# Kernel optimization log

Measured on AMD Instinct MI355X. Metric: run time of the kernel, lower is better.

The kernel has to match this reference:

```python
import jax, jax.numpy as jnp
import numpy as np

KH = KW = 3
K = KH * KW
STRIDE = 1
PAD = 1
DIL = 1
DG = 1  # deformable groups


def conv2d(x, w, b):
    out = jax.lax.conv_general_dilated(
        x, w, window_strides=(STRIDE, STRIDE),
        padding=[(PAD, PAD), (PAD, PAD)], rhs_dilation=(DIL, DIL),
        dimension_numbers=('NCHW', 'OIHW', 'NCHW'))
    return out + b[None, :, None, None]


def deform_conv2d(x, offset, mask, w, b):
    """DCNv2: bilinear sample at predicted offsets, modulate by mask, GEMM with w."""
    B, Cin, H, W = x.shape
    Ho, Wo = offset.shape[2], offset.shape[3]
    cpg = Cin // DG
    # torchvision layout: channel 2*(g*K+k) = dy, 2*(g*K+k)+1 = dx
    off = offset.reshape(B, DG, K, 2, Ho, Wo)
    off_y, off_x = off[:, :, :, 0], off[:, :, :, 1]  # [B,DG,K,Ho,Wo]
    m = mask.reshape(B, DG, K, Ho, Wo)
    ky = jnp.repeat(jnp.arange(KH), KW) * DIL          # [K] kernel row offsets
    kx = jnp.tile(jnp.arange(KW), KH) * DIL            # [K] kernel col offsets
    hh = jnp.arange(Ho) * STRIDE - PAD
    ww = jnp.arange(Wo) * STRIDE - PAD
    py = off_y + ky[None, None, :, None, None] + hh[None, None, None, :, None]
    px = off_x + kx[None, None, :, None, None] + ww[None, None, None, None, :]
    y0 = jnp.floor(py); x0 = jnp.floor(px)
    wy = py - y0; wx = px - x0
    x_g = x.reshape(B, DG, cpg, H * W)

    def gather(yc, xc):  # zero-padded bilinear corner fetch
        valid = ((yc >= 0) & (yc < H) & (xc >= 0) & (xc < W)).astype(x.dtype)
        yi = jnp.clip(yc, 0, H - 1).astype(jnp.int32)
        xi = jnp.clip(xc, 0, W - 1).astype(jnp.int32)
        idx = (yi * W + xi).reshape(B, DG, 1, K * Ho * Wo)
        v = jnp.take_along_axis(x_g, jnp.broadcast_to(idx, (B, DG, cpg, K * Ho * Wo)), axis=3)
        return v.reshape(B, DG, cpg, K, Ho, Wo) * valid[:, :, None]

    v00 = gather(y0, x0)
    v01 = gather(y0, x0 + 1)
    v10 = gather(y0 + 1, x0)
    v11 = gather(y0 + 1, x0 + 1)
    wy_b = wy[:, :, None]; wx_b = wx[:, :, None]  # broadcast over cpg
    sampled = (v00 * (1 - wy_b) * (1 - wx_b) + v01 * (1 - wy_b) * wx_b
               + v10 * wy_b * (1 - wx_b) + v11 * wy_b * wx_b)
    sampled = (sampled * m[:, :, None]).reshape(B, Cin, K, Ho, Wo)
    Cout = w.shape[0]
    out = jnp.einsum('bckhw,ock->bohw', sampled, w.reshape(Cout, Cin, K))
    return out + b[None, :, None, None]


def setup_inputs() -> dict:
    key = jax.random.key(0)
    k1, k2, k3, k4 = jax.random.split(key, 4)
    B, Cin, Cout, H, W = 8, 128, 128, 64, 64
    omc = DG * 3 * K  # 2*K offsets + K mask channels = 27
    x = jax.random.normal(k1, (B, Cin, H, W), dtype=jnp.float32)
    # small offset-conv weights -> modest predicted offsets (mimics near-zero init)
    w_off = jax.random.normal(k2, (omc, Cin, KH, KW), dtype=jnp.float32) * 0.01
    b_off = jnp.zeros((omc,), dtype=jnp.float32)
    w_def = jax.random.normal(k3, (Cout, Cin, KH, KW), dtype=jnp.float32) * (1.0 / np.sqrt(Cin * K))
    b_def = jax.random.normal(k4, (Cout,), dtype=jnp.float32) * 0.01
    return {"x": x, "w_off": w_off, "b_off": b_off, "w_def": w_def, "b_def": b_def}


def reference(x, w_off, b_off, w_def, b_def):
    out = conv2d(x, w_off, b_off)
    oc = DG * 2 * K
    offset = out[:, :oc]
    mask = jax.nn.sigmoid(out[:, oc:])
    return deform_conv2d(x, offset, mask, w_def, b_def)
```

## Files before the change

kernel.cpp:

```cpp
#include <hip/hip_runtime.h>
#include <math.h>

typedef _Float16 f16;
typedef __attribute__((ext_vector_type(2))) _Float16 f16x2;
typedef __attribute__((ext_vector_type(4))) _Float16 f16x4;
typedef __attribute__((ext_vector_type(8))) _Float16 f16x8;
typedef __attribute__((ext_vector_type(4))) float f32x4;

#define NBATCH 8
#define WSA_ELE 36864
#define WSB_ELE 147456
#define PREP_BLOCKS 720
#define OFF_WSB  73728
#define OFF_XT   368640

#define WIN_OFF    0
#define A_OFF      131072
#define SOFF_OFF   147456
#define SMEM_BYTES 161536

__device__ __forceinline__ void gload_lds16(const f16* gsrc, f16* ldst) {
  __builtin_amdgcn_global_load_lds(
      (const __attribute__((address_space(1))) unsigned int*)gsrc,
      (__attribute__((address_space(3))) unsigned int*)ldst, 16, 0, 0);
}

__global__ __launch_bounds__(256) void prep_transpose_kernel(const float* __restrict__ w_off,
                                                             const float* __restrict__ w_def,
                                                             f16* __restrict__ wsA,
                                                             f16* __restrict__ wsB,
                                                             const float* __restrict__ x,
                                                             f16* __restrict__ xt) {
  __shared__ __align__(16) f16 s_t[128 * 68];
  const int t = threadIdx.x;
  if (blockIdx.x < PREP_BLOCKS) {
    int i = blockIdx.x * 256 + t;
    if (i < WSA_ELE) {
      int j = i & 7, lane = (i >> 3) & 63, fm = i >> 9;
      int ch = fm >> 1, mt = fm & 1;
      int row = mt * 16 + (lane & 15);
      int kidx = ch * 32 + (lane >> 4) * 8 + j;
      int k = kidx >> 7, cc = kidx & 127;
      float v = (row < 27) ? w_off[row * 1152 + cc * 9 + k] : 0.0f;
      wsA[i] = (f16)v;
    } else {
      int e = i - WSA_ELE;
      int j = e & 7, lane = (e >> 3) & 63, fm = e >> 9;
      int ch = fm >> 3, mt = fm & 7;
      int row = mt * 16 + (lane & 15);
      int kidx = ch * 32 + (lane >> 4) * 8 + j;
      int k = kidx >> 7, cc = kidx & 127;
      wsB[e] = (f16)w_def[row * 1152 + cc * 9 + k];
    }
    return;
  }
  const int bid = blockIdx.x - PREP_BLOCKS;
  const int b = bid >> 6;
  const int pos0 = (bid & 63) << 6;
  const float* xb = x + ((size_t)b << 19);
  #pragma unroll
  for (int it = 0; it < 8; ++it) {
    int i = it * 256 + t;
    int c = i >> 4, p4 = (i & 15) << 2;
    float4 v = *(const float4*)&xb[c * 4096 + pos0 + p4];
    f16x4 h = {(f16)v.x, (f16)v.y, (f16)v.z, (f16)v.w};
    *(f16x4*)&s_t[c * 68 + p4] = h;
  }
  __syncthreads();
  f16* xtb = xt + ((size_t)b << 19);
  #pragma unroll
  for (int it = 0; it < 8; ++it) {
    int i = it * 256 + t;
    int p = i >> 5, c4 = (i & 31) << 2;
    f16x4 h = {s_t[(c4    ) * 68 + p],
               s_t[(c4 + 1) * 68 + p],
               s_t[(c4 + 2) * 68 + p],
               s_t[(c4 + 3) * 68 + p]};
    *(f16x4*)&xtb[(size_t)(pos0 + p) * 128 + c4] = h;
  }
}

__global__ __launch_bounds__(512, 1) void fused_dcn_kernel(const f16* __restrict__ xt,
                                                           const f16* __restrict__ wsA,
                                                           const f16* __restrict__ wsB,
                                                           const float* __restrict__ b_off,
                                                           const float* __restrict__ b_def,
                                                           float* __restrict__ out) {
  extern __shared__ __align__(16) char smem[];
  char*  win      = smem;
  f16*   s_a      = (f16*)(smem + A_OFF);
  float* s_offall = (float*)(smem + SOFF_OFF);

  const int t = threadIdx.x;
  const int b = blockIdx.x & 7;
  const int hp = blockIdx.x >> 3;
  const int lane = t & 63, wid = t >> 6;
  const int row = wid >> 2;
  const int rowy = hp * 2 + row;
  const int q = lane >> 4, li = lane & 15;
  const int px = ((wid & 3) << 4) + li;
  const char* xtb = (const char*)xt + ((size_t)b << 20);
  const int y_lo = max(hp * 2 - 3, 0);
  const int y_hi = min(hp * 2 + 4, 63);

  {
    const int nunits = (y_hi - y_lo + 1) << 10;
    for (int u = t; u < nunits; u += 512) {
      const int r = u >> 10, rem = u & 1023;
      const int xx = rem >> 4, s = rem & 15;
      const int qq = s & 3, cc4 = s >> 2;
      const uint4 v = *(const uint4*)(xtb + ((((y_lo + r) * 64 + xx) << 8) + (cc4 << 6) + (qq << 4)));
      const int s1 = xx & 3, s2 = (xx >> 2) & 1;
      *(uint4*)(win + (((r * 64 + xx) << 8) + ((qq ^ s1) << 4) + ((cc4 ^ s2) << 6))) = v;
    }
  }
  __syncthreads();

  {
    float* so = s_offall + row * (27 * 65);
    f32x4 acc0 = {0.f, 0.f, 0.f, 0.f}, acc1 = {0.f, 0.f, 0.f, 0.f};
    #pragma unroll
    for (int k = 0; k < 9; ++k) {
      const int ky = k / 3, kx = k - ky * 3;
      const int y = rowy + ky - 1;
      const int xx = px + kx - 1;
      const bool valid = ((unsigned)y < 64u) && ((unsigned)xx < 64u);
      const int yc = min(max(y, y_lo), y_hi);
      const int xc = min(max(xx, 0), 63);
      const int base = (((yc - y_lo) * 64 + xc) << 8) + ((q ^ (xc & 3)) << 4) + ((((xc >> 2) & 1)) << 6);
      #pragma unroll
      for (int c4 = 0; c4 < 4; ++c4) {
        union { uint4 u; f16x8 v; } bu;
        bu.u = *(const uint4*)(win + (base ^ (c4 << 6)));
        if (!valid) { bu.u.x = 0u; bu.u.y = 0u; bu.u.z = 0u; bu.u.w = 0u; }
        const int ch = k * 4 + c4;
        f16x8 a0 = *(const f16x8*)&wsA[(ch * 2    ) * 512 + lane * 8];
        f16x8 a1 = *(const f16x8*)&wsA[(ch * 2 + 1) * 512 + lane * 8];
        acc0 = __builtin_amdgcn_mfma_f32_16x16x32_f16(a0, bu.v, acc0, 0, 0, 0);
        acc1 = __builtin_amdgcn_mfma_f32_16x16x32_f16(a1, bu.v, acc1, 0, 0, 0);
      }
    }
    #pragma unroll
    for (int mt = 0; mt < 2; ++mt) {
      f32x4 a = mt ? acc1 : acc0;
      #pragma unroll
      for (int r = 0; r < 4; ++r) {
        int oc = mt * 16 + q * 4 + r;
        if (oc < 27) {
          float v = a[r] + b_off[oc];
          if (oc >= 18) v = 1.0f / (1.0f + __expf(-v));
          so[oc * 65 + px] = v;
        }
      }
    }
  }
  __syncthreads();

  unsigned posA[9], posB[9];
  f16x4 wts[9];
  {
    const float* so = s_offall + row * (27 * 65);
    #pragma unroll
    for (int k = 0; k < 9; ++k) {
      const int ky = k / 3, kx = k - ky * 3;
      float oy = so[(2 * k    ) * 65 + px];
      float ox = so[(2 * k + 1) * 65 + px];
      float m  = so[(18 + k   ) * 65 + px];
      float py  = oy + (float)(rowy + ky - 1);
      float pxf = ox + (float)(px + kx - 1);
      float y0f = floorf(py), x0f = floorf(pxf);
      float wy = py - y0f, wx = pxf - x0f;
      int y0 = (int)y0f, x0 = (int)x0f;
      bool y0v = (unsigned)y0 < 64u, y1v = (unsigned)(y0 + 1) < 64u;
      bool x0v = (unsigned)x0 < 64u, x1v = (unsigned)(x0 + 1) < 64u;
      int y0a = min(max(y0, y_lo), y_hi), y1a = min(max(y0 + 1, y_lo), y_hi);
      int x0c = min(max(x0, 0), 63),      x1c = min(max(x0 + 1, 0), 63);
      unsigned i00 = (unsigned)((y0a - y_lo) * 64 + x0c);
      unsigned i01 = (unsigned)((y0a - y_lo) * 64 + x1c);
      unsigned i10 = (unsigned)((y1a - y_lo) * 64 + x0c);
      unsigned i11 = (unsigned)((y1a - y_lo) * 64 + x1c);
      posA[k] = i00 | (i01 << 16);
      posB[k] = i10 | (i11 << 16);
      float w0 = (y0v && x0v) ? (1.f - wy) * (1.f - wx) * m : 0.f;
      float w1 = (y0v && x1v) ? (1.f - wy) * wx         * m : 0.f;
      float w2 = (y1v && x0v) ? wy         * (1.f - wx) * m : 0.f;
      float w3 = (y1v && x1v) ? wy         * wx         * m : 0.f;
      f16x4 wp = {(f16)w0, (f16)w1, (f16)w2, (f16)w3};
      wts[k] = wp;
    }
  }

  gload_lds16(wsB + wid * 512 + lane * 8, s_a + wid * 512);
  __syncthreads();

  f32x4 acc[8];
  #pragma unroll
  for (int mt = 0; mt < 8; ++mt) acc[mt] = (f32x4){0.f, 0.f, 0.f, 0.f};

  #pragma unroll
  for (int k = 0; k < 9; ++k) {
    const unsigned wA = posA[k], wB = posB[k];
    const unsigned i00 = wA & 0xFFFFu, i01 = wA >> 16;
    const unsigned i10 = wB & 0xFFFFu, i11 = wB >> 16;
    const int b00 = (int)((i00 << 8) + (((unsigned)q ^ (i00 & 3)) << 4) + (((i00 >> 2) & 1) << 6));
    const int b01 = (int)((i01 << 8) + (((unsigned)q ^ (i01 & 3)) << 4) + (((i01 >> 2) & 1) << 6));
    const int b10 = (int)((i10 << 8) + (((unsigned)q ^ (i10 & 3)) << 4) + (((i10 >> 2) & 1) << 6));
    const int b11 = (int)((i11 << 8) + (((unsigned)q ^ (i11 & 3)) << 4) + (((i11 >> 2) & 1) << 6));
    const f16x4 wv = wts[k];
    const f16x2 wp0 = {wv.x, wv.x}, wp1 = {wv.y, wv.y};
    const f16x2 wp2 = {wv.z, wv.z}, wp3 = {wv.w, wv.w};
    #pragma unroll
    for (int c4 = 0; c4 < 4; ++c4) {
      const int ch = k * 4 + c4;
      if (ch < 35)
        gload_lds16(wsB + (ch + 1) * 4096 + wid * 512 + lane * 8,
                    s_a + ((ch + 1) & 1) * 4096 + wid * 512);
      const int cx = c4 << 6;
      union { uint4 u; f16x2 h[4]; } d0, d1, d2, d3;
      d0.u = *(const uint4*)(win + (b00 ^ cx));
      d1.u = *(const uint4*)(win + (b01 ^ cx));
      d2.u = *(const uint4*)(win + (b10 ^ cx));
      d3.u = *(const uint4*)(win + (b11 ^ cx));
      union { f16x2 h[4]; f16x8 v; } bf;
      #pragma unroll
      for (int i = 0; i < 4; ++i) {
        f16x2 s = d0.h[i] * wp0;
        s = s + d1.h[i] * wp1;
        s = s + d2.h[i] * wp2;
        s = s + d3.h[i] * wp3;
        bf.h[i] = s;
      }
      const f16* ab = s_a + (ch & 1) * 4096;
      #pragma unroll
      for (int mt = 0; mt < 8; ++mt) {
        f16x8 a = *(const f16x8*)&ab[mt * 512 + lane * 8];
        acc[mt] = __builtin_amdgcn_mfma_f32_16x16x32_f16(a, bf.v, acc[mt], 0, 0, 0);
      }
      __syncthreads();
    }
  }

  float* o = out + (size_t)b * 128 * 4096 + rowy * 64 + px;
  #pragma unroll
  for (int mt = 0; mt < 8; ++mt) {
    #pragma unroll
    for (int r = 0; r < 4; ++r) {
      int oc = mt * 16 + q * 4 + r;
      o[oc * 4096] = acc[mt][r] + b_def[oc];
    }
  }
}

extern "C" void kernel_launch(void* const* d_in, const int* in_sizes, int n_in,
                              void* d_out, int out_size, void* d_ws, size_t ws_size,
                              hipStream_t stream) {
  const float* x     = (const float*)d_in[0];
  const float* w_off = (const float*)d_in[1];
  const float* b_off = (const float*)d_in[2];
  const float* w_def = (const float*)d_in[3];
  const float* b_def = (const float*)d_in[4];
  float* out = (float*)d_out;

  f16* wsA = (f16*)d_ws;
  f16* wsB = (f16*)((char*)d_ws + OFF_WSB);
  f16* xt  = (f16*)((char*)d_ws + OFF_XT);

  static int smem_opted = 0;
  if (!smem_opted) {
    hipFuncSetAttribute((const void*)fused_dcn_kernel,
                        hipFuncAttributeMaxDynamicSharedMemorySize, SMEM_BYTES);
    smem_opted = 1;
  }

  prep_transpose_kernel<<<dim3(PREP_BLOCKS + NBATCH * 64), dim3(256), 0, stream>>>(
      w_off, w_def, wsA, wsB, x, xt);
  fused_dcn_kernel<<<dim3(NBATCH * 32), dim3(512), SMEM_BYTES, stream>>>(
      xt, wsA, wsB, b_off, b_def, out);
}
```

Measured before the change: 111.7 us.

## Fuse NCHW-to-NHWC fp16 transpose into main DCN kernel window load

Removes the separate x transpose pass and its global fp16 intermediate. The main kernel now reads fp32 NCHW rows directly, converts them to fp16, and transposes them through an LDS scratch tile into the swizzled window. The scratch region is shared with the offset buffer and the weight staging area to cut LDS use, which needs an extra barrier. The cost is that each block re-reads and re-transposes up to 8 overlapping rows, and each row goes through two barriers serially with little overlap.

```diff
diff --git a/kernel.cpp b/kernel.cpp
--- a/kernel.cpp
+++ b/kernel.cpp
@@ -12,12 +12,10 @@
 #define WSB_ELE 147456
 #define PREP_BLOCKS 720
 #define OFF_WSB  73728
-#define OFF_XT   368640
 
 #define WIN_OFF    0
-#define A_OFF      131072
-#define SOFF_OFF   147456
-#define SMEM_BYTES 161536
+#define SCR_OFF    131072
+#define SMEM_BYTES 148480
 
 __device__ __forceinline__ void gload_lds16(const f16* gsrc, f16* ldst) {
   __builtin_amdgcn_global_load_lds(
@@ -25,71 +23,41 @@
       (__attribute__((address_space(3))) unsigned int*)ldst, 16, 0, 0);
 }
 
-__global__ __launch_bounds__(256) void prep_transpose_kernel(const float* __restrict__ w_off,
-                                                             const float* __restrict__ w_def,
-                                                             f16* __restrict__ wsA,
-                                                             f16* __restrict__ wsB,
-                                                             const float* __restrict__ x,
-                                                             f16* __restrict__ xt) {
-  __shared__ __align__(16) f16 s_t[128 * 68];
-  const int t = threadIdx.x;
-  if (blockIdx.x < PREP_BLOCKS) {
-    int i = blockIdx.x * 256 + t;
-    if (i < WSA_ELE) {
-      int j = i & 7, lane = (i >> 3) & 63, fm = i >> 9;
-      int ch = fm >> 1, mt = fm & 1;
-      int row = mt * 16 + (lane & 15);
-      int kidx = ch * 32 + (lane >> 4) * 8 + j;
-      int k = kidx >> 7, cc = kidx & 127;
-      float v = (row < 27) ? w_off[row * 1152 + cc * 9 + k] : 0.0f;
-      wsA[i] = (f16)v;
-    } else {
-      int e = i - WSA_ELE;
-      int j = e & 7, lane = (e >> 3) & 63, fm = e >> 9;
-      int ch = fm >> 3, mt = fm & 7;
-      int row = mt * 16 + (lane & 15);
-      int kidx = ch * 32 + (lane >> 4) * 8 + j;
-      int k = kidx >> 7, cc = kidx & 127;
-      wsB[e] = (f16)w_def[row * 1152 + cc * 9 + k];
-    }
-    return;
-  }
-  const int bid = blockIdx.x - PREP_BLOCKS;
-  const int b = bid >> 6;
-  const int pos0 = (bid & 63) << 6;
-  const float* xb = x + ((size_t)b << 19);
-  #pragma unroll
-  for (int it = 0; it < 8; ++it) {
-    int i = it * 256 + t;
-    int c = i >> 4, p4 = (i & 15) << 2;
-    float4 v = *(const float4*)&xb[c * 4096 + pos0 + p4];
-    f16x4 h = {(f16)v.x, (f16)v.y, (f16)v.z, (f16)v.w};
-    *(f16x4*)&s_t[c * 68 + p4] = h;
-  }
-  __syncthreads();
-  f16* xtb = xt + ((size_t)b << 19);
-  #pragma unroll
-  for (int it = 0; it < 8; ++it) {
-    int i = it * 256 + t;
-    int p = i >> 5, c4 = (i & 31) << 2;
-    f16x4 h = {s_t[(c4    ) * 68 + p],
-               s_t[(c4 + 1) * 68 + p],
-               s_t[(c4 + 2) * 68 + p],
-               s_t[(c4 + 3) * 68 + p]};
-    *(f16x4*)&xtb[(size_t)(pos0 + p) * 128 + c4] = h;
-  }
-}
-
-__global__ __launch_bounds__(512, 1) void fused_dcn_kernel(const f16* __restrict__ xt,
+__global__ __launch_bounds__(256) void prep_w_kernel(const float* __restrict__ w_off,
+                                                     const float* __restrict__ w_def,
+                                                     f16* __restrict__ wsA,
+                                                     f16* __restrict__ wsB) {
+  int i = blockIdx.x * 256 + threadIdx.x;
+  if (i < WSA_ELE) {
+    int j = i & 7, lane = (i >> 3) & 63, fm = i >> 9;
+    int ch = fm >> 1, mt = fm & 1;
+    int row = mt * 16 + (lane & 15);
+    int kidx = ch * 32 + (lane >> 4) * 8 + j;
+    int k = kidx >> 7, cc = kidx & 127;
+    float v = (row < 27) ? w_off[row * 1152 + cc * 9 + k] : 0.0f;
+    wsA[i] = (f16)v;
+  } else {
+    int e = i - WSA_ELE;
+    int j = e & 7, lane = (e >> 3) & 63, fm = e >> 9;
+    int ch = fm >> 3, mt = fm & 7;
+    int row = mt * 16 + (lane & 15);
+    int kidx = ch * 32 + (lane >> 4) * 8 + j;
+    int k = kidx >> 7, cc = kidx & 127;
+    wsB[e] = (f16)w_def[row * 1152 + cc * 9 + k];
+  }
+}
+
+__global__ __launch_bounds__(512, 1) void fused_dcn_kernel(const float* __restrict__ x,
                                                            const f16* __restrict__ wsA,
                                                            const f16* __restrict__ wsB,
                                                            const float* __restrict__ b_off,
                                                            const float* __restrict__ b_def,
                                                            float* __restrict__ out) {
   extern __shared__ __align__(16) char smem[];
-  char*  win      = smem;
-  f16*   s_a      = (f16*)(smem + A_OFF);
-  float* s_offall = (float*)(smem + SOFF_OFF);
+  char*  win      = smem + WIN_OFF;
+  f16*   tile     = (f16*)(smem + SCR_OFF);
+  float* s_offall = (float*)(smem + SCR_OFF);
+  f16*   s_a      = (f16*)(smem + SCR_OFF);
 
   const int t = threadIdx.x;
   const int b = blockIdx.x & 7;
@@ -99,22 +67,35 @@
   const int rowy = hp * 2 + row;
   const int q = lane >> 4, li = lane & 15;
   const int px = ((wid & 3) << 4) + li;
-  const char* xtb = (const char*)xt + ((size_t)b << 20);
   const int y_lo = max(hp * 2 - 3, 0);
   const int y_hi = min(hp * 2 + 4, 63);
-
-  {
-    const int nunits = (y_hi - y_lo + 1) << 10;
-    for (int u = t; u < nunits; u += 512) {
-      const int r = u >> 10, rem = u & 1023;
-      const int xx = rem >> 4, s = rem & 15;
-      const int qq = s & 3, cc4 = s >> 2;
-      const uint4 v = *(const uint4*)(xtb + ((((y_lo + r) * 64 + xx) << 8) + (cc4 << 6) + (qq << 4)));
-      const int s1 = xx & 3, s2 = (xx >> 2) & 1;
-      *(uint4*)(win + (((r * 64 + xx) << 8) + ((qq ^ s1) << 4) + ((cc4 ^ s2) << 6))) = v;
-    }
-  }
-  __syncthreads();
+  const int nrows = y_hi - y_lo + 1;
+  const float* xb = x + ((size_t)b << 19);
+
+  for (int rr = 0; rr < nrows; ++rr) {
+    const int y = y_lo + rr;
+    #pragma unroll
+    for (int i2 = 0; i2 < 4; ++i2) {
+      int it = i2 * 512 + t;
+      int c = it >> 4, g4 = (it & 15) << 2;
+      float4 v = *(const float4*)&xb[c * 4096 + y * 64 + g4];
+      f16x4 hh = {(f16)v.x, (f16)v.y, (f16)v.z, (f16)v.w};
+      *(f16x4*)&tile[c * 68 + g4] = hh;
+    }
+    __syncthreads();
+    #pragma unroll
+    for (int j = 0; j < 2; ++j) {
+      int u = j * 512 + t;
+      int xx = u >> 4, s = u & 15;
+      int qq = s & 3, cc4 = s >> 2;
+      union { f16 h[8]; uint4 u4; } bu;
+      #pragma unroll
+      for (int d = 0; d < 8; ++d) bu.h[d] = tile[(s * 8 + d) * 68 + xx];
+      int s1 = xx & 3, s2 = (xx >> 2) & 1;
+      *(uint4*)(win + (((rr * 64 + xx) << 8) + ((qq ^ s1) << 4) + ((cc4 ^ s2) << 6))) = bu.u4;
+    }
+    __syncthreads();
+  }
 
   {
     float* so = s_offall + row * (27 * 65);
@@ -189,6 +170,7 @@
       wts[k] = wp;
     }
   }
+  __syncthreads();
 
   gload_lds16(wsB + wid * 512 + lane * 8, s_a + wid * 512);
   __syncthreads();
@@ -263,7 +245,6 @@
 
   f16* wsA = (f16*)d_ws;
   f16* wsB = (f16*)((char*)d_ws + OFF_WSB);
-  f16* xt  = (f16*)((char*)d_ws + OFF_XT);
 
   static int smem_opted = 0;
   if (!smem_opted) {
@@ -272,8 +253,7 @@
     smem_opted = 1;
   }
 
-  prep_transpose_kernel<<<dim3(PREP_BLOCKS + NBATCH * 64), dim3(256), 0, stream>>>(
-      w_off, w_def, wsA, wsB, x, xt);
+  prep_w_kernel<<<dim3(PREP_BLOCKS), dim3(256), 0, stream>>>(w_off, w_def, wsA, wsB);
   fused_dcn_kernel<<<dim3(NBATCH * 32), dim3(512), SMEM_BYTES, stream>>>(
-      xt, wsA, wsB, b_off, b_def, out);
-}
+      x, wsA, wsB, b_off, b_def, out);
+}
```

Measured after the change: 114.5 us. +2.5%, slower.
